# Kernel tuning notes

Measured on AMD Instinct MI355X. Metric: run time of the kernel, lower is better.

The kernel has to match this reference:

```python
import jax, jax.numpy as jnp
import numpy as np

DIM = 128
IN_DIM = 2
LAYERS = 4
H = 256
W = 256
WH = W // 2 + 1  # rfft last-dim size
RATIO = 1.0


def _radial_mask():
    # waves = sqrt(k^2 + r^2) over the rfft2 grid; keep waves <= (W//2)*ratio
    k = np.fft.rfftfreq(W) * W            # (WH,)
    r = np.fft.fftfreq(H) * H             # (H,)
    waves = np.sqrt(k[None, :] ** 2 + r[:, None] ** 2)  # (H, WH)
    return jnp.asarray(waves <= (W // 2) * RATIO)


def conv1x1(x, w, b):
    # x: (b,c,h,w), w: (o,c), b: (o,)
    return jnp.einsum('bchw,oc->bohw', x, w) + b[None, :, None, None]


def setup_inputs() -> dict:
    key = jax.random.key(0)
    ks = jax.random.split(key, 15)
    d = DIM
    inp = {
        'x': jax.random.normal(ks[0], (4, IN_DIM, H, W), dtype=jnp.float32),
        'enc_w': jax.random.normal(ks[1], (d, IN_DIM), dtype=jnp.float32) * (1.0 / np.sqrt(IN_DIM)),
        'enc_b': jnp.zeros((d,), dtype=jnp.float32),
        'pos_emb': jax.random.normal(ks[2], (1, d, H, W), dtype=jnp.float32) * 0.02,
        'mlp_w1': jax.random.normal(ks[3], (LAYERS, 4 * d, d), dtype=jnp.float32) * (1.0 / np.sqrt(d)),
        'mlp_b1': jnp.zeros((LAYERS, 4 * d), dtype=jnp.float32),
        'mlp_w2': jax.random.normal(ks[4], (LAYERS, d, 4 * d), dtype=jnp.float32) * (1.0 / np.sqrt(4 * d)),
        'mlp_b2': jnp.zeros((LAYERS, d), dtype=jnp.float32),
        'spec_mags': jax.random.normal(ks[5], (LAYERS, d, H, WH), dtype=jnp.float32),
        'spec_phases': jax.random.normal(ks[6], (LAYERS, d, H, WH), dtype=jnp.float32),
        'oxo_w': jax.random.normal(ks[7], (LAYERS, d, d), dtype=jnp.float32) * (1.0 / np.sqrt(d)),
        'oxo_b': jnp.zeros((LAYERS, d), dtype=jnp.float32),
        'dec_w': jax.random.normal(ks[8], (IN_DIM, d), dtype=jnp.float32) * (1.0 / np.sqrt(d)),
        'dec_b': jnp.zeros((IN_DIM,), dtype=jnp.float32),
    }
    return inp


def reference(x, enc_w, enc_b, pos_emb, mlp_w1, mlp_b1, mlp_w2, mlp_b2,
              spec_mags, spec_phases, oxo_w, oxo_b, dec_w, dec_b):
    scale = (DIM / IN_DIM) ** 0.5
    mask = _radial_mask()  # (H, WH) bool, constant
    h = conv1x1(x, enc_w, enc_b) * scale + pos_emb
    for i in range(LAYERS):
        # mlp block: 1x1 conv -> SiLU -> 1x1 conv
        x1 = jax.nn.silu(conv1x1(h, mlp_w1[i], mlp_b1[i]))
        x1 = conv1x1(x1, mlp_w2[i], mlp_b2[i])
        # spectral conv: rfft2 (ortho), complex filter on radially-masked modes,
        # zeros elsewhere (equivalent to masked_select/scatter in the original), irfft2
        xf = jnp.fft.rfft2(x1, norm='ortho')  # (b,c,H,WH) complex64
        filt = jax.nn.sigmoid(spec_mags[i]) * jnp.exp(1j * spec_phases[i])  # (c,H,WH)
        xf = jnp.where(mask[None, None, :, :], xf * filt[None], 0.0 + 0.0j)
        x1 = jnp.fft.irfft2(xf, s=(H, W), norm='ortho')
        x1 = conv1x1(x1, oxo_w[i], oxo_b[i])
        h = x1 + h
    return conv1x1(h, dec_w, dec_b) / scale
```

## Files before the change

### kernel.cpp

```cpp
#include <hip/hip_runtime.h>
#include <math.h>

#define PI2 6.2831853071795864769f

typedef short bf16x8 __attribute__((ext_vector_type(8)));
typedef float f32x4 __attribute__((ext_vector_type(4)));
typedef int   i32x4 __attribute__((ext_vector_type(4)));
typedef unsigned short ushort_t;

__device__ inline unsigned splitf(float v) {
    unsigned u  = __float_as_uint(v);
    unsigned r  = (u + 0x7fffu + ((u >> 16) & 1u)) >> 16;
    float hi    = __uint_as_float(r << 16);
    float lof   = v - hi;
    unsigned u2 = __float_as_uint(lof);
    unsigned r2 = (u2 + 0x7fffu + ((u2 >> 16) & 1u)) >> 16;
    return (r & 0xffffu) | (r2 << 16);
}
__device__ inline float upk(unsigned w) {
    return __uint_as_float(w << 16) + __uint_as_float(w & 0xffff0000u);
}

union VecU { i32x4 i; bf16x8 s; };

__device__ inline void unpack2(i32x4 d0, i32x4 d1, bf16x8& hi, bf16x8& lo) {
    VecU h, l;
    h.i.x = __builtin_amdgcn_perm(d0.y, d0.x, 0x05040100);
    h.i.y = __builtin_amdgcn_perm(d0.w, d0.z, 0x05040100);
    h.i.z = __builtin_amdgcn_perm(d1.y, d1.x, 0x05040100);
    h.i.w = __builtin_amdgcn_perm(d1.w, d1.z, 0x05040100);
    l.i.x = __builtin_amdgcn_perm(d0.y, d0.x, 0x07060302);
    l.i.y = __builtin_amdgcn_perm(d0.w, d0.z, 0x07060302);
    l.i.z = __builtin_amdgcn_perm(d1.y, d1.x, 0x07060302);
    l.i.w = __builtin_amdgcn_perm(d1.w, d1.z, 0x07060302);
    hi = h.s; lo = l.s;
}

__device__ inline void unpack8(const int* d, bf16x8& hi, bf16x8& lo) {
    VecU h, l;
    h.i.x = __builtin_amdgcn_perm(d[1], d[0], 0x05040100);
    h.i.y = __builtin_amdgcn_perm(d[3], d[2], 0x05040100);
    h.i.z = __builtin_amdgcn_perm(d[5], d[4], 0x05040100);
    h.i.w = __builtin_amdgcn_perm(d[7], d[6], 0x05040100);
    l.i.x = __builtin_amdgcn_perm(d[1], d[0], 0x07060302);
    l.i.y = __builtin_amdgcn_perm(d[3], d[2], 0x07060302);
    l.i.z = __builtin_amdgcn_perm(d[5], d[4], 0x07060302);
    l.i.w = __builtin_amdgcn_perm(d[7], d[6], 0x07060302);
    hi = h.s; lo = l.s;
}

__global__ void sentinel_kernel(float* __restrict__ out, int n) {
    int t = blockIdx.x * 256 + threadIdx.x;
    if (t < n) out[t] = 12345.0f;
}

__global__ void split_kernel(const float* __restrict__ in, unsigned* __restrict__ out) {
    long q = (long)blockIdx.x * 256 + threadIdx.x;
    const float4* ip = (const float4*)in;
    float4 v = ip[q];
    i32x4 o;
    o.x = (int)splitf(v.x); o.y = (int)splitf(v.y);
    o.z = (int)splitf(v.z); o.w = (int)splitf(v.w);
    ((i32x4*)out)[q] = o;
}

__global__ void split_planes_kernel(const float* __restrict__ in,
                                    ushort_t* __restrict__ hi, ushort_t* __restrict__ lo) {
    long q = (long)blockIdx.x * 256 + threadIdx.x;
    float4 v = ((const float4*)in)[q];
    unsigned s0 = splitf(v.x), s1 = splitf(v.y), s2 = splitf(v.z), s3 = splitf(v.w);
    uint2 hw, lw;
    hw.x = (s0 & 0xffffu) | (s1 << 16);
    hw.y = (s2 & 0xffffu) | (s3 << 16);
    lw.x = (s0 >> 16) | (s1 & 0xffff0000u);
    lw.y = (s2 >> 16) | (s3 & 0xffff0000u);
    *(uint2*)(hi + q * 4) = hw;
    *(uint2*)(lo + q * 4) = lw;
}

__global__ void enc_kernel(const float* __restrict__ x, const float* __restrict__ w,
                           const float* __restrict__ b, const float* __restrict__ pos,
                           unsigned* __restrict__ h) {
    long t = (long)blockIdx.x * 256 + threadIdx.x;
    int pq = (int)(t & 16383);
    int c  = (int)((t >> 14) & 127);
    int bb = (int)(t >> 21);
    float4 x0 = *(const float4*)(x + ((long)bb * 2 + 0) * 65536 + pq * 4);
    float4 x1 = *(const float4*)(x + ((long)bb * 2 + 1) * 65536 + pq * 4);
    float4 pv = *(const float4*)(pos + (long)c * 65536 + pq * 4);
    float w0 = w[c * 2], w1 = w[c * 2 + 1], bc = b[c];
    uint4 o;
    o.x = splitf((w0 * x0.x + w1 * x1.x + bc) * 8.0f + pv.x);
    o.y = splitf((w0 * x0.y + w1 * x1.y + bc) * 8.0f + pv.y);
    o.z = splitf((w0 * x0.z + w1 * x1.z + bc) * 8.0f + pv.z);
    o.w = splitf((w0 * x0.w + w1 * x1.w + bc) * 8.0f + pv.w);
    *(uint4*)(h + t * 4) = o;
}

__global__ __launch_bounds__(256, 2)
void mlp_fused(const unsigned* __restrict__ Ax,
               const ushort_t* __restrict__ W1hi, const ushort_t* __restrict__ W1lo,
               const float* __restrict__ b1,
               const ushort_t* __restrict__ W2hi, const ushort_t* __restrict__ W2lo,
               const float* __restrict__ b2, float* __restrict__ t2) {
    __shared__ unsigned SM[13312];
    ushort_t* Ahi = (ushort_t*)SM;
    ushort_t* Alo = Ahi + 64 * 136;
    ushort_t* Hhi = Alo + 64 * 136;
    ushort_t* Hlo = Hhi + 64 * 72;
    int tid = threadIdx.x;
    int w = tid >> 6, l = tid & 63;
    int lr = l & 15, lg = l >> 4;
    int p0 = blockIdx.x * 64;

#pragma unroll
    for (int i = 0; i < 8; i++) {
        int f = i * 256 + tid;
        int k = f >> 4, q = f & 15;
        uint4 v = *(const uint4*)(Ax + (long)k * 65536 + p0 + q * 4);
        int px = q * 4;
        Ahi[(px + 0) * 136 + k] = (ushort_t)v.x;  Alo[(px + 0) * 136 + k] = (ushort_t)(v.x >> 16);
        Ahi[(px + 1) * 136 + k] = (ushort_t)v.y;  Alo[(px + 1) * 136 + k] = (ushort_t)(v.y >> 16);
        Ahi[(px + 2) * 136 + k] = (ushort_t)v.z;  Alo[(px + 2) * 136 + k] = (ushort_t)(v.z >> 16);
        Ahi[(px + 3) * 136 + k] = (ushort_t)v.w;  Alo[(px + 3) * 136 + k] = (ushort_t)(v.w >> 16);
    }
    __syncthreads();

    f32x4 acc2[4][2] = {};
#pragma unroll 1
    for (int c = 0; c < 8; c++) {
        f32x4 acc1[4] = {};
#pragma unroll
        for (int ks = 0; ks < 4; ks++) {
            long boff = (long)(c * 64 + w * 16 + lr) * 128 + ks * 32 + lg * 8;
            bf16x8 bh = *(const bf16x8*)(W1hi + boff);
            bf16x8 bl = *(const bf16x8*)(W1lo + boff);
#pragma unroll
            for (int ms = 0; ms < 4; ms++) {
                int aoff = (ms * 16 + lr) * 136 + ks * 32 + lg * 8;
                bf16x8 ah = *(const bf16x8*)&Ahi[aoff];
                bf16x8 al = *(const bf16x8*)&Alo[aoff];
                acc1[ms] = __builtin_amdgcn_mfma_f32_16x16x32_bf16(ah, bh, acc1[ms], 0, 0, 0);
                acc1[ms] = __builtin_amdgcn_mfma_f32_16x16x32_bf16(ah, bl, acc1[ms], 0, 0, 0);
                acc1[ms] = __builtin_amdgcn_mfma_f32_16x16x32_bf16(al, bh, acc1[ms], 0, 0, 0);
            }
        }
        {
            int hl = w * 16 + lr;
            float bias = b1[c * 64 + hl];
#pragma unroll
            for (int ms = 0; ms < 4; ms++)
#pragma unroll
                for (int r = 0; r < 4; r++) {
                    float pre = acc1[ms][r] + bias;
                    float s = pre / (1.0f + __expf(-pre));
                    unsigned sp = splitf(s);
                    int pix = ms * 16 + lg * 4 + r;
                    Hhi[pix * 72 + hl] = (ushort_t)sp;
                    Hlo[pix * 72 + hl] = (ushort_t)(sp >> 16);
                }
        }
        __syncthreads();
#pragma unroll
        for (int ks2 = 0; ks2 < 2; ks2++) {
            bf16x8 bh[2], bl[2];
#pragma unroll
            for (int ns = 0; ns < 2; ns++) {
                long boff = (long)(w * 32 + ns * 16 + lr) * 512 + c * 64 + ks2 * 32 + lg * 8;
                bh[ns] = *(const bf16x8*)(W2hi + boff);
                bl[ns] = *(const bf16x8*)(W2lo + boff);
            }
#pragma unroll
            for (int ms = 0; ms < 4; ms++) {
                int hoff = (ms * 16 + lr) * 72 + ks2 * 32 + lg * 8;
                bf16x8 ah = *(const bf16x8*)&Hhi[hoff];
                bf16x8 al = *(const bf16x8*)&Hlo[hoff];
#pragma unroll
                for (int ns = 0; ns < 2; ns++) {
                    acc2[ms][ns] = __builtin_amdgcn_mfma_f32_16x16x32_bf16(ah, bh[ns], acc2[ms][ns], 0, 0, 0);
                    acc2[ms][ns] = __builtin_amdgcn_mfma_f32_16x16x32_bf16(ah, bl[ns], acc2[ms][ns], 0, 0, 0);
                    acc2[ms][ns] = __builtin_amdgcn_mfma_f32_16x16x32_bf16(al, bh[ns], acc2[ms][ns], 0, 0, 0);
                }
            }
        }
        __syncthreads();
    }
    float* T = (float*)SM;
#pragma unroll
    for (int ns = 0; ns < 2; ns++) {
        int n = w * 32 + ns * 16 + lr;
        float bias = b2[n];
#pragma unroll
        for (int ms = 0; ms < 4; ms++)
#pragma unroll
            for (int r = 0; r < 4; r++) {
                int pix = ms * 16 + lg * 4 + r;
                T[n * 68 + pix] = acc2[ms][ns][r] + bias;
            }
    }
    __syncthreads();
#pragma unroll
    for (int i = 0; i < 8; i++) {
        int f = i * 256 + tid;
        int n = f >> 4, q = f & 15;
        float4 v = *(const float4*)&T[n * 68 + q * 4];
        *(float4*)(t2 + (long)n * 65536 + p0 + q * 4) = v;
    }
}

__global__ __launch_bounds__(256, 2)
void oxo_kernel(const unsigned* __restrict__ Tx, const unsigned* __restrict__ Bx,
                const float* __restrict__ ob, unsigned* __restrict__ h) {
    __shared__ float T[128 * 128];
    int tid = threadIdx.x;
    int w = tid >> 6, l = tid & 63;
    int lr = l & 15, lg = l >> 4;
    int m0 = blockIdx.x * 128;
    int n0 = w * 32;
    f32x4 acc[8][2] = {};
    for (int k0 = 0; k0 < 128; k0 += 32) {
        bf16x8 bh[2], bl[2];
#pragma unroll
        for (int ns = 0; ns < 2; ns++) {
            const unsigned* bp = Bx + (n0 + ns * 16 + lr) * 128 + k0 + lg * 8;
            i32x4 d0 = *(const i32x4*)bp;
            i32x4 d1 = *(const i32x4*)(bp + 4);
            unpack2(d0, d1, bh[ns], bl[ns]);
        }
#pragma unroll
        for (int ms = 0; ms < 8; ms++) {
            const unsigned* ap = Tx + (long)(k0 + lg * 8) * 65536 + m0 + ms * 16 + lr;
            int d[8];
#pragma unroll
            for (int j = 0; j < 8; j++) d[j] = (int)ap[(long)j * 65536];
            bf16x8 ah, al; unpack8(d, ah, al);
#pragma unroll
            for (int ns = 0; ns < 2; ns++) {
                acc[ms][ns] = __builtin_amdgcn_mfma_f32_16x16x32_bf16(ah, bh[ns], acc[ms][ns], 0, 0, 0);
                acc[ms][ns] = __builtin_amdgcn_mfma_f32_16x16x32_bf16(ah, bl[ns], acc[ms][ns], 0, 0, 0);
                acc[ms][ns] = __builtin_amdgcn_mfma_f32_16x16x32_bf16(al, bh[ns], acc[ms][ns], 0, 0, 0);
            }
        }
    }
#pragma unroll
    for (int ns = 0; ns < 2; ns++) {
        int n = n0 + ns * 16 + lr;
#pragma unroll
        for (int ms = 0; ms < 8; ms++) {
            int blk = ((ms * 4 + lg) + n) & 31;
#pragma unroll
            for (int r = 0; r < 4; r++)
                T[n * 128 + blk * 4 + r] = acc[ms][ns][r];
        }
    }
    __syncthreads();
#pragma unroll
    for (int i = 0; i < 16; i++) {
        int flat = i * 256 + tid;
        int n = flat >> 5, q = flat & 31;
        const float4* src = (const float4*)&T[n * 128 + (((q + n) & 31) * 4)];
        float4 v = *src;
        float bias = ob[n];
        unsigned* hp = h + (long)n * 65536 + m0 + q * 4;
        uint4 hv = *(uint4*)hp;
        uint4 o;
        o.x = splitf(upk(hv.x) + v.x + bias);
        o.y = splitf(upk(hv.y) + v.y + bias);
        o.z = splitf(upk(hv.z) + v.z + bias);
        o.w = splitf(upk(hv.w) + v.w + bias);
        *(uint4*)hp = o;
    }
}

__global__ void fft_row_fwd(const float* __restrict__ in, float2* __restrict__ freq, int c0) {
    __shared__ float2 A[4][256];
    __shared__ float2 B[4][256];
    __shared__ float2 TW[128];
    int tid = threadIdx.x;
    int img = blockIdx.x >> 6, rgrp = blockIdx.x & 63;
    if (tid < 128) {
        float sn, cs; __sincosf((PI2 / 256.f) * (float)tid, &sn, &cs);
        TW[tid] = make_float2(cs, sn);
    }
    {
        int r = tid >> 6, l = tid & 63;
        const float4* src = (const float4*)(in + ((long)(c0 + img) * 256 + rgrp * 4 + r) * 256);
        float4 v = src[l];
        A[r][l * 4 + 0] = make_float2(v.x, 0.f);
        A[r][l * 4 + 1] = make_float2(v.y, 0.f);
        A[r][l * 4 + 2] = make_float2(v.z, 0.f);
        A[r][l * 4 + 3] = make_float2(v.w, 0.f);
    }
    __syncthreads();
    float2 (*s)[256] = A; float2 (*d)[256] = B;
    for (int m = 1; m < 256; m <<= 1) {
#pragma unroll
        for (int q = 0; q < 2; q++) {
            int bf = tid + q * 256;
            int r = bf >> 7, i = bf & 127;
            int jm = i & ~(m - 1);
            float2 c0v = s[r][i], c1 = s[r][i + 128];
            float2 t = TW[jm];
            float2 df = make_float2(c0v.x - c1.x, c0v.y - c1.y);
            d[r][i + jm]     = make_float2(c0v.x + c1.x, c0v.y + c1.y);
            d[r][i + jm + m] = make_float2(t.x * df.x + t.y * df.y, t.x * df.y - t.y * df.x);
        }
        __syncthreads();
        float2 (*tmp)[256] = s; s = d; d = tmp;
    }
    long ib = (long)img * 34816;
    for (int q = tid; q < 4 * 129; q += 256) {
        int r = q / 129; int k = q - r * 129;
        freq[ib + (k >> 3) * 2048 + (rgrp * 4 + r) * 8 + (k & 7)] = s[r][k];
    }
}

__global__ void fft_col(float2* __restrict__ freq, const float* __restrict__ mags,
                        const float* __restrict__ phases, int c0) {
    __shared__ float2 A[8][256];
    __shared__ float2 B[8][256];
    __shared__ float2 TW[128];
    int tid = threadIdx.x;
    int img = blockIdx.x / 17;
    int kt  = blockIdx.x % 17;
    int kx0 = kt * 8;
    float2* base = freq + (long)img * 34816 + kt * 2048;
    if (tid < 128) {
        float sn, cs; __sincosf((PI2 / 256.f) * (float)tid, &sn, &cs);
        TW[tid] = make_float2(cs, sn);
    }
#pragma unroll
    for (int q = 0; q < 8; q++) {
        int e = tid + q * 256;
        A[e & 7][e >> 3] = base[e];
    }
    __syncthreads();
    float2 (*s)[256] = A; float2 (*d)[256] = B;
    for (int m = 1; m < 256; m <<= 1) {
#pragma unroll
        for (int q = 0; q < 4; q++) {
            int bf = tid + q * 256;
            int cl = bf >> 7, i = bf & 127;
            int jm = i & ~(m - 1);
            float2 c0v = s[cl][i], c1 = s[cl][i + 128];
            float2 t = TW[jm];
            float2 df = make_float2(c0v.x - c1.x, c0v.y - c1.y);
            d[cl][i + jm]     = make_float2(c0v.x + c1.x, c0v.y + c1.y);
            d[cl][i + jm + m] = make_float2(t.x * df.x + t.y * df.y, t.x * df.y - t.y * df.x);
        }
        __syncthreads();
        float2 (*tmp)[256] = s; s = d; d = tmp;
    }
#pragma unroll
    for (int q = 0; q < 8; q++) {
        int e = tid + q * 256;
        int cl = e & 7, ky = e >> 3;
        int kx = kx0 + cl;
        float2 v = s[cl][ky];
        float2 r = make_float2(0.f, 0.f);
        if (kx < 129) {
            int ry = ky < 128 ? ky : ky - 256;
            if (kx * kx + ry * ry <= 16384) {
                long fi = ((long)(c0 + img) * 256 + ky) * 129 + kx;
                float mg = mags[fi], ph = phases[fi];
                float sg = 1.0f / (1.0f + __expf(-mg));
                float sn, cs; __sincosf(ph, &sn, &cs);
                float fr = sg * cs, fim = sg * sn;
                r = make_float2(v.x * fr - v.y * fim, v.x * fim + v.y * fr);
            }
        }
        s[cl][ky] = r;
    }
    __syncthreads();
    for (int m = 1; m < 256; m <<= 1) {
#pragma unroll
        for (int q = 0; q < 4; q++) {
            int bf = tid + q * 256;
            int cl = bf >> 7, i = bf & 127;
            int jm = i & ~(m - 1);
            float2 c0v = s[cl][i], c1 = s[cl][i + 128];
            float2 t = TW[jm];
            float2 df = make_float2(c0v.x - c1.x, c0v.y - c1.y);
            d[cl][i + jm]     = make_float2(c0v.x + c1.x, c0v.y + c1.y);
            d[cl][i + jm + m] = make_float2(t.x * df.x - t.y * df.y, t.x * df.y + t.y * df.x);
        }
        __syncthreads();
        float2 (*tmp)[256] = s; s = d; d = tmp;
    }
#pragma unroll
    for (int q = 0; q < 8; q++) {
        int e = tid + q * 256;
        base[e] = s[e & 7][e >> 3];
    }
}

__global__ void fft_row_inv(const float2* __restrict__ freq, unsigned* __restrict__ out, int c0) {
    __shared__ float2 A[4][256];
    __shared__ float2 B[4][256];
    __shared__ float2 TW[128];
    int tid = threadIdx.x;
    int img = blockIdx.x >> 6, rgrp = blockIdx.x & 63;
    if (tid < 128) {
        float sn, cs; __sincosf((PI2 / 256.f) * (float)tid, &sn, &cs);
        TW[tid] = make_float2(cs, sn);
    }
    long ib = (long)img * 34816;
#pragma unroll
    for (int q = 0; q < 4; q++) {
        int e = tid + q * 256;
        int r = e >> 8, xx = e & 255;
        int k = (xx <= 128) ? xx : 256 - xx;
        float2 v = freq[ib + (k >> 3) * 2048 + (rgrp * 4 + r) * 8 + (k & 7)];
        if (xx > 128) v.y = -v.y;
        A[r][xx] = v;
    }
    __syncthreads();
    float2 (*s)[256] = A; float2 (*d)[256] = B;
    for (int m = 1; m < 256; m <<= 1) {
#pragma unroll
        for (int q = 0; q < 2; q++) {
            int bf = tid + q * 256;
            int r = bf >> 7, i = bf & 127;
            int jm = i & ~(m - 1);
            float2 c0v = s[r][i], c1 = s[r][i + 128];
            float2 t = TW[jm];
            float2 df = make_float2(c0v.x - c1.x, c0v.y - c1.y);
            d[r][i + jm]     = make_float2(c0v.x + c1.x, c0v.y + c1.y);
            d[r][i + jm + m] = make_float2(t.x * df.x - t.y * df.y, t.x * df.y + t.y * df.x);
        }
        __syncthreads();
        float2 (*tmp)[256] = s; s = d; d = tmp;
    }
    {
        int r = tid >> 6, l = tid & 63;
        const float sc = 1.0f / 65536.0f;
        uint4 o;
        o.x = splitf(s[r][l * 4 + 0].x * sc);
        o.y = splitf(s[r][l * 4 + 1].x * sc);
        o.z = splitf(s[r][l * 4 + 2].x * sc);
        o.w = splitf(s[r][l * 4 + 3].x * sc);
        *(uint4*)(out + ((long)(c0 + img) * 256 + rgrp * 4 + r) * 256 + l * 4) = o;
    }
}

__global__ void dec_kernel(const unsigned* __restrict__ h, const float* __restrict__ w,
                           const float* __restrict__ b, float* __restrict__ out) {
    int t = blockIdx.x * 256 + threadIdx.x;
    int bb = t >> 16, p = t & 65535;
    const unsigned* hb = h + (long)bb * 8388608 + p;
    float a0 = b[0], a1 = b[1];
    float a0b = 0.f, a1b = 0.f;
#pragma unroll 4
    for (int c = 0; c < 128; c += 2) {
        float h0 = upk(hb[(long)c * 65536]);
        float h1 = upk(hb[(long)(c + 1) * 65536]);
        a0  += w[c] * h0;        a1  += w[128 + c] * h0;
        a0b += w[c + 1] * h1;    a1b += w[128 + c + 1] * h1;
    }
    out[((long)bb * 2 + 0) * 65536 + p] = (a0 + a0b) * 0.125f;
    out[((long)bb * 2 + 1) * 65536 + p] = (a1 + a1b) * 0.125f;
}

extern "C" void kernel_launch(void* const* d_in, const int* in_sizes, int n_in,
                              void* d_out, int out_size, void* d_ws, size_t ws_size,
                              hipStream_t stream) {
    const float* x        = (const float*)d_in[0];
    const float* enc_w    = (const float*)d_in[1];
    const float* enc_b    = (const float*)d_in[2];
    const float* pos_emb  = (const float*)d_in[3];
    const float* mlp_w1   = (const float*)d_in[4];
    const float* mlp_b1   = (const float*)d_in[5];
    const float* mlp_w2   = (const float*)d_in[6];
    const float* mlp_b2   = (const float*)d_in[7];
    const float* spec_mag = (const float*)d_in[8];
    const float* spec_ph  = (const float*)d_in[9];
    const float* oxo_w    = (const float*)d_in[10];
    const float* oxo_b    = (const float*)d_in[11];
    const float* dec_w    = (const float*)d_in[12];
    const float* dec_b    = (const float*)d_in[13];
    float* outp = (float*)d_out;

    const size_t WS_NEEDED = 186187776ULL;
    if (ws_size < WS_NEEDED) {
        sentinel_kernel<<<(out_size + 255) / 256, 256, 0, stream>>>(outp, out_size);
        return;
    }

    unsigned* u    = (unsigned*)d_ws;
    unsigned* h    = u;
    float*    t2   = (float*)(u + 33554432);
    unsigned* TxO  = (unsigned*)t2;
    float2*   freq = (float2*)(u + 41943040);
    unsigned* Wx1  = u + 46399488;
    unsigned* Wx2  = Wx1 + 65536;
    unsigned* Wox  = Wx2 + 65536;
    ushort_t* W1hi = (ushort_t*)Wx1;
    ushort_t* W1lo = (ushort_t*)(Wx1 + 32768);
    ushort_t* W2hi = (ushort_t*)Wx2;
    ushort_t* W2lo = (ushort_t*)(Wx2 + 32768);

    enc_kernel<<<32768, 256, 0, stream>>>(x, enc_w, enc_b, pos_emb, h);

    for (int l = 0; l < 4; l++) {
        split_planes_kernel<<<64, 256, 0, stream>>>(mlp_w1 + (long)l * 65536, W1hi, W1lo);
        split_planes_kernel<<<64, 256, 0, stream>>>(mlp_w2 + (long)l * 65536, W2hi, W2lo);
        split_kernel<<<16, 256, 0, stream>>>(oxo_w + (long)l * 16384, Wox);
        const float* b1l = mlp_b1 + l * 512;
        const float* b2l = mlp_b2 + l * 128;
        const float* mgl = spec_mag + (long)l * 4227072;
        const float* phl = spec_ph  + (long)l * 4227072;
        const float* obl = oxo_b + l * 128;
        for (int b = 0; b < 4; b++) {
            unsigned* hb = h + (long)b * 8388608;
            mlp_fused<<<1024, 256, 0, stream>>>(hb, W1hi, W1lo, b1l, W2hi, W2lo, b2l, t2);
            for (int c0 = 0; c0 < 128; c0 += 64) {
                fft_row_fwd<<<4096, 256, 0, stream>>>(t2, freq, c0);
                fft_col<<<64 * 17, 256, 0, stream>>>(freq, mgl, phl, c0);
                fft_row_inv<<<4096, 256, 0, stream>>>(freq, TxO, c0);
            }
            oxo_kernel<<<512, 256, 0, stream>>>(TxO, Wox, obl, hb);
        }
    }

    dec_kernel<<<1024, 256, 0, stream>>>(h, dec_w, dec_b, outp);
}
```

Before: 4.048 ms.

## Halve MLP pixel tile, swizzle LDS layout, and use lighter LDS barriers

Shrinks the fused MLP block tile from 64 to 32 pixels, doubles the grid, halves shared memory and raises the launch-bounds occupancy target from 2 to 4 blocks. Adds an XOR swizzle on the K index in the A and H LDS tiles to reduce bank conflicts on transposed stores and MFMA operand loads. Replaces __syncthreads with a barrier that waits only on LDS counters. Smaller tiles mean each block reloads the W1/W2 weight fragments for half as many pixels, which raises global/L2 weight traffic per pixel.

```diff
diff --git a/kernel.cpp b/kernel.cpp
--- a/kernel.cpp
+++ b/kernel.cpp
@@ -48,6 +48,12 @@
     l.i.w = __builtin_amdgcn_perm(d[7], d[6], 0x07060302);
     hi = h.s; lo = l.s;
 }
+
+#define LBAR() do { \
+    asm volatile("s_waitcnt lgkmcnt(0)" ::: "memory"); \
+    __builtin_amdgcn_s_barrier(); \
+    asm volatile("" ::: "memory"); \
+} while (0)
 
 __global__ void sentinel_kernel(float* __restrict__ out, int n) {
     int t = blockIdx.x * 256 + threadIdx.x;
@@ -97,47 +103,49 @@
     *(uint4*)(h + t * 4) = o;
 }
 
-__global__ __launch_bounds__(256, 2)
+__global__ __launch_bounds__(256, 4)
 void mlp_fused(const unsigned* __restrict__ Ax,
                const ushort_t* __restrict__ W1hi, const ushort_t* __restrict__ W1lo,
                const float* __restrict__ b1,
                const ushort_t* __restrict__ W2hi, const ushort_t* __restrict__ W2lo,
                const float* __restrict__ b2, float* __restrict__ t2) {
-    __shared__ unsigned SM[13312];
+    __shared__ unsigned SM[6656];
     ushort_t* Ahi = (ushort_t*)SM;
-    ushort_t* Alo = Ahi + 64 * 136;
-    ushort_t* Hhi = Alo + 64 * 136;
-    ushort_t* Hlo = Hhi + 64 * 72;
+    ushort_t* Alo = Ahi + 32 * 136;
+    ushort_t* Hhi = Alo + 32 * 136;
+    ushort_t* Hlo = Hhi + 32 * 72;
     int tid = threadIdx.x;
     int w = tid >> 6, l = tid & 63;
     int lr = l & 15, lg = l >> 4;
-    int p0 = blockIdx.x * 64;
-
-#pragma unroll
-    for (int i = 0; i < 8; i++) {
+    int p0 = blockIdx.x * 32;
+
+#pragma unroll
+    for (int i = 0; i < 4; i++) {
         int f = i * 256 + tid;
-        int k = f >> 4, q = f & 15;
+        int k = f >> 3, q = f & 7;
         uint4 v = *(const uint4*)(Ax + (long)k * 65536 + p0 + q * 4);
+        int kk = k ^ (q << 3);
         int px = q * 4;
-        Ahi[(px + 0) * 136 + k] = (ushort_t)v.x;  Alo[(px + 0) * 136 + k] = (ushort_t)(v.x >> 16);
-        Ahi[(px + 1) * 136 + k] = (ushort_t)v.y;  Alo[(px + 1) * 136 + k] = (ushort_t)(v.y >> 16);
-        Ahi[(px + 2) * 136 + k] = (ushort_t)v.z;  Alo[(px + 2) * 136 + k] = (ushort_t)(v.z >> 16);
-        Ahi[(px + 3) * 136 + k] = (ushort_t)v.w;  Alo[(px + 3) * 136 + k] = (ushort_t)(v.w >> 16);
-    }
-    __syncthreads();
-
-    f32x4 acc2[4][2] = {};
+        Ahi[(px + 0) * 136 + kk] = (ushort_t)v.x;  Alo[(px + 0) * 136 + kk] = (ushort_t)(v.x >> 16);
+        Ahi[(px + 1) * 136 + kk] = (ushort_t)v.y;  Alo[(px + 1) * 136 + kk] = (ushort_t)(v.y >> 16);
+        Ahi[(px + 2) * 136 + kk] = (ushort_t)v.z;  Alo[(px + 2) * 136 + kk] = (ushort_t)(v.z >> 16);
+        Ahi[(px + 3) * 136 + kk] = (ushort_t)v.w;  Alo[(px + 3) * 136 + kk] = (ushort_t)(v.w >> 16);
+    }
+    LBAR();
+
+    f32x4 acc2[2][2] = {};
 #pragma unroll 1
     for (int c = 0; c < 8; c++) {
-        f32x4 acc1[4] = {};
+        f32x4 acc1[2] = {};
 #pragma unroll
         for (int ks = 0; ks < 4; ks++) {
             long boff = (long)(c * 64 + w * 16 + lr) * 128 + ks * 32 + lg * 8;
             bf16x8 bh = *(const bf16x8*)(W1hi + boff);
             bf16x8 bl = *(const bf16x8*)(W1lo + boff);
 #pragma unroll
-            for (int ms = 0; ms < 4; ms++) {
-                int aoff = (ms * 16 + lr) * 136 + ks * 32 + lg * 8;
+            for (int ms = 0; ms < 2; ms++) {
+                int px = ms * 16 + lr;
+                int aoff = px * 136 + ((ks * 32 + lg * 8) ^ (((px >> 2) & 7) << 3));
                 bf16x8 ah = *(const bf16x8*)&Ahi[aoff];
                 bf16x8 al = *(const bf16x8*)&Alo[aoff];
                 acc1[ms] = __builtin_amdgcn_mfma_f32_16x16x32_bf16(ah, bh, acc1[ms], 0, 0, 0);
@@ -149,18 +157,19 @@
             int hl = w * 16 + lr;
             float bias = b1[c * 64 + hl];
 #pragma unroll
-            for (int ms = 0; ms < 4; ms++)
+            for (int ms = 0; ms < 2; ms++)
 #pragma unroll
                 for (int r = 0; r < 4; r++) {
                     float pre = acc1[ms][r] + bias;
                     float s = pre / (1.0f + __expf(-pre));
                     unsigned sp = splitf(s);
                     int pix = ms * 16 + lg * 4 + r;
-                    Hhi[pix * 72 + hl] = (ushort_t)sp;
-                    Hlo[pix * 72 + hl] = (ushort_t)(sp >> 16);
+                    int hk = hl ^ (((pix >> 2) & 7) << 3);
+                    Hhi[pix * 72 + hk] = (ushort_t)sp;
+                    Hlo[pix * 72 + hk] = (ushort_t)(sp >> 16);
                 }
         }
-        __syncthreads();
+        LBAR();
 #pragma unroll
         for (int ks2 = 0; ks2 < 2; ks2++) {
             bf16x8 bh[2], bl[2];
@@ -171,8 +180,9 @@
                 bl[ns] = *(const bf16x8*)(W2lo + boff);
             }
 #pragma unroll
-            for (int ms = 0; ms < 4; ms++) {
-                int hoff = (ms * 16 + lr) * 72 + ks2 * 32 + lg * 8;
+            for (int ms = 0; ms < 2; ms++) {
+                int pix = ms * 16 + lr;
+                int hoff = pix * 72 + ((ks2 * 32 + lg * 8) ^ (((pix >> 2) & 7) << 3));
                 bf16x8 ah = *(const bf16x8*)&Hhi[hoff];
                 bf16x8 al = *(const bf16x8*)&Hlo[hoff];
 #pragma unroll
@@ -183,7 +193,7 @@
                 }
             }
         }
-        __syncthreads();
+        LBAR();
     }
     float* T = (float*)SM;
 #pragma unroll
@@ -191,19 +201,19 @@
         int n = w * 32 + ns * 16 + lr;
         float bias = b2[n];
 #pragma unroll
-        for (int ms = 0; ms < 4; ms++)
+        for (int ms = 0; ms < 2; ms++)
 #pragma unroll
             for (int r = 0; r < 4; r++) {
                 int pix = ms * 16 + lg * 4 + r;
-                T[n * 68 + pix] = acc2[ms][ns][r] + bias;
-            }
-    }
-    __syncthreads();
-#pragma unroll
-    for (int i = 0; i < 8; i++) {
+                T[n * 36 + pix] = acc2[ms][ns][r] + bias;
+            }
+    }
+    LBAR();
+#pragma unroll
+    for (int i = 0; i < 4; i++) {
         int f = i * 256 + tid;
-        int n = f >> 4, q = f & 15;
-        float4 v = *(const float4*)&T[n * 68 + q * 4];
+        int n = f >> 3, q = f & 7;
+        float4 v = *(const float4*)&T[n * 36 + q * 4];
         *(float4*)(t2 + (long)n * 65536 + p0 + q * 4) = v;
     }
 }
@@ -512,7 +522,7 @@
         const float* obl = oxo_b + l * 128;
         for (int b = 0; b < 4; b++) {
             unsigned* hb = h + (long)b * 8388608;
-            mlp_fused<<<1024, 256, 0, stream>>>(hb, W1hi, W1lo, b1l, W2hi, W2lo, b2l, t2);
+            mlp_fused<<<2048, 256, 0, stream>>>(hb, W1hi, W1lo, b1l, W2hi, W2lo, b2l, t2);
             for (int c0 = 0; c0 < 128; c0 += 64) {
                 fft_row_fwd<<<4096, 256, 0, stream>>>(t2, freq, c0);
                 fft_col<<<64 * 17, 256, 0, stream>>>(freq, mgl, phl, c0);
```

Measured after the change: 4.538 ms. 12.1% more time.
